# Optimization experiments

Measured on AMD Instinct MI355X. Metric: run time of the kernel, lower is better.

Reference implementation:

```python
import jax, jax.numpy as jnp
import numpy as np

B, N, V, D, L = 8, 2048, 256, 512, 6
H, DH = 8, 64
INNER = H * DH          # 512
WSZ = 128               # local attention window
NW = N // WSZ           # 16 windows (N multiple of WSZ -> autopad no-op)
FF = int(D * 4 * 2 / 3) # 1365 GEGLU inner dim
SCALE = DH ** -0.5
DPB = D // 2            # dynamic position bias MLP width


def _ln(x, g, b):
    m = x.mean(-1, keepdims=True)
    v = ((x - m) ** 2).mean(-1, keepdims=True)
    return (x - m) * jax.lax.rsqrt(v + 1e-5) * g + b


def _pos_emb(n, d):
    inv = 1.0 / (10000.0 ** (jnp.arange(0, d, 2, dtype=jnp.float32) / d))
    s = jnp.arange(n, dtype=jnp.float32)[:, None] * inv[None, :]
    return jnp.concatenate([jnp.sin(s), jnp.cos(s)], axis=-1)  # (n, d)


def _look(t, pad_val):
    # t: (..., NW, WSZ, c) -> (..., NW, 2*WSZ, c): [previous window, current window]
    prev = jnp.concatenate([jnp.full_like(t[..., :1, :, :], pad_val), t[..., :-1, :, :]], axis=-3)
    return jnp.concatenate([prev, t], axis=-2)


def _dpb_bias(w1, b1, w2, b2, w3, b3):
    # DynamicPositionBias(i=WSZ, j=2*WSZ) -> (H, WSZ, 2*WSZ)
    rel = jnp.arange(2 * WSZ, dtype=jnp.float32)[:, None]
    h = jax.nn.silu(rel @ w1 + b1)
    h = jax.nn.silu(h @ w2 + b2)
    tab = h @ w3 + b3                       # (2*WSZ, H)
    iseq = jnp.arange(WSZ, 2 * WSZ)
    jseq = jnp.arange(2 * WSZ)
    idx = jnp.abs(iseq[:, None] - jseq[None, :])  # (WSZ, 2*WSZ)
    return jnp.transpose(tab[idx], (2, 0, 1))


def setup_inputs():
    key = jax.random.key(0)
    ks = jax.random.split(key, 12)
    nrm = lambda k, shape, s=0.02: jax.random.normal(k, shape, dtype=jnp.float32) * s
    emb = nrm(ks[1], (V, D), 1.0).at[0].set(0.0)  # padding_idx=0 row zeroed
    return dict(
        x=jax.random.randint(ks[0], (B, N), 0, V),
        emb=emb,
        ln_attn_g=jnp.ones((L, D)), ln_attn_b=jnp.zeros((L, D)),
        w_qkv=nrm(ks[2], (L, D, 3 * INNER)),
        w_out=nrm(ks[3], (L, INNER, D)),
        ln_ff_g=jnp.ones((L, D)), ln_ff_b=jnp.zeros((L, D)),
        w_ff1=nrm(ks[4], (L, D, 2 * FF)),
        w_ff2=nrm(ks[5], (L, FF, D)),
        dpb_w1=nrm(ks[6], (1, DPB), 0.5), dpb_b1=jnp.zeros((DPB,)),
        dpb_w2=nrm(ks[7], (DPB, DPB), 0.05), dpb_b2=jnp.zeros((DPB,)),
        dpb_w3=nrm(ks[8], (DPB, H), 0.05), dpb_b3=jnp.zeros((H,)),
        ln_out_g=jnp.ones((D,)), ln_out_b=jnp.zeros((D,)),
        w_logits=nrm(ks[9], (D, D)),
    )


def _forward(x, emb, ln_attn_g, ln_attn_b, w_qkv, w_out, ln_ff_g, ln_ff_b,
             w_ff1, w_ff2, dpb_w1, dpb_b1, dpb_w2, dpb_b2, dpb_w3, dpb_b3,
             ln_out_g, ln_out_b, w_logits):
    mask = x != 0                                  # padding mask (B, N)
    h = emb[x] * mask[..., None] + _pos_emb(N, D)[None]
    bias = _dpb_bias(dpb_w1, dpb_b1, dpb_w2, dpb_b2, dpb_w3, dpb_b3)  # (H, w, 2w)
    pos = jnp.arange(N).reshape(NW, WSZ)
    kpos = _look(pos[None, :, :, None], -1)[0, :, :, 0]               # (NW, 2w)
    # causal mask + exact-windowsize clip + left pad mask (shared over batch/heads)
    inval = (pos[:, :, None] < kpos[:, None, :]) | (pos[:, :, None] > kpos[:, None, :] + WSZ) | (kpos[:, None, :] == -1)
    kmask = _look(mask.reshape(B, NW, WSZ)[..., None], False)[..., 0]  # (B, NW, 2w)
    neg = -jnp.finfo(jnp.float32).max

    def towin(t):  # (B, N, INNER) -> (B, H, NW, WSZ, DH)
        return t.reshape(B, N, H, DH).transpose(0, 2, 1, 3).reshape(B, H, NW, WSZ, DH)

    def layer(hx, p):
        lg, lb, wqkv, wout, fg, fb, w1, w2 = p
        # local windowed attention: look_backward=1, look_forward=0, causal
        z = _ln(hx, lg, lb)
        q, k, v = map(towin, jnp.split(z @ wqkv, 3, axis=-1))
        k2, v2 = _look(k, -1.0), _look(v, -1.0)   # pad_value=-1 (masked below)
        sim = jnp.einsum('bhwid,bhwjd->bhwij', q * SCALE, k2) + bias[None, :, None]
        sim = jnp.where(inval[None, None], neg, sim)
        sim = jnp.where(kmask[:, None, :, None, :], sim, neg)
        a = jax.nn.softmax(sim, axis=-1)
        o = jnp.einsum('bhwij,bhwjd->bhwid', a, v2)
        o = o.reshape(B, H, N, DH).transpose(0, 2, 1, 3).reshape(B, N, INNER)
        hx = hx + o @ wout
        # GEGLU feed-forward
        u = _ln(hx, fg, fb) @ w1
        a1, g1 = jnp.split(u, 2, axis=-1)
        hx = hx + (a1 * jax.nn.gelu(g1, approximate=False)) @ w2
        return hx, None

    h, _ = jax.lax.scan(layer, h, (ln_attn_g, ln_attn_b, w_qkv, w_out, ln_ff_g, ln_ff_b, w_ff1, w_ff2))
    return _ln(h, ln_out_g, ln_out_b) @ w_logits   # (B, N, D)


def reference(x, emb, ln_attn_g, ln_attn_b, w_qkv, w_out, ln_ff_g, ln_ff_b,
              w_ff1, w_ff2, dpb_w1, dpb_b1, dpb_w2, dpb_b2, dpb_w3, dpb_b3,
              ln_out_g, ln_out_b, w_logits):
    return _forward(x, emb, ln_attn_g, ln_attn_b, w_qkv, w_out, ln_ff_g, ln_ff_b,
                    w_ff1, w_ff2, dpb_w1, dpb_b1, dpb_w2, dpb_b2, dpb_w3, dpb_b3,
                    ln_out_g, ln_out_b, w_logits)
```

## Files before the change

### kernel.cpp

```cpp
#include <hip/hip_runtime.h>
#include <hip/hip_bf16.h>
#include <math.h>

typedef __hip_bfloat16 bf16;
typedef __attribute__((ext_vector_type(8))) short short8;
typedef __attribute__((ext_vector_type(4))) float floatx4;

#define NEG_MAX 3.402823466e38f

__device__ __forceinline__ void gload16(const void* g, void* l) {
  __builtin_amdgcn_global_load_lds(
      (const __attribute__((address_space(1))) unsigned int*)g,
      (__attribute__((address_space(3))) unsigned int*)l, 16, 0, 0);
}
__device__ __forceinline__ floatx4 mfma_bf16(short8 a, short8 b, floatx4 c) {
  return __builtin_amdgcn_mfma_f32_16x16x32_bf16(a, b, c, 0, 0, 0);
}

__global__ __launch_bounds__(256) void prep_w(const float* __restrict__ src,
                                              bf16* __restrict__ dst,
                                              int K, int N, int pK, int pN, int nl, int mode) {
  int idx = blockIdx.x * 256 + threadIdx.x;
  long total = (long)nl * pN * pK;
  if (idx >= total) return;
  int l = idx / (pN * pK);
  int r = idx % (pN * pK);
  int n = r / pK, k = r % pK;
  const float* s = src + (size_t)l * K * N;
  float v = 0.f;
  if (k < K) {
    int sc = -1;
    if (mode == 0) { if (n < N) sc = n; }
    else { if (n < 1365) sc = n; else if (n >= 1408 && n < 2773) sc = 1365 + (n - 1408); }
    if (sc >= 0) v = s[(size_t)k * N + sc];
  }
  dst[idx] = __float2bfloat16(v);
}

__global__ __launch_bounds__(256) void dpb_kernel(const float* w1, const float* b1,
                                                  const float* w2, const float* b2,
                                                  const float* w3, const float* b3,
                                                  float* __restrict__ tab) {
  __shared__ float h1[256];
  __shared__ float h2s[256];
  int t = blockIdx.x, e = threadIdx.x;
  float rel = (float)t;
  float a = rel * w1[e] + b1[e];
  h1[e] = a / (1.f + expf(-a));
  __syncthreads();
  float s = b2[e];
  for (int d = 0; d < 256; d++) s += h1[d] * w2[d * 256 + e];
  h2s[e] = s / (1.f + expf(-s));
  __syncthreads();
  if (e < 8) {
    float s2 = b3[e];
    for (int d = 0; d < 256; d++) s2 += h2s[d] * w3[d * 8 + e];
    tab[t * 8 + e] = s2;
  }
}

__global__ __launch_bounds__(256) void embed_kernel(const int* __restrict__ x,
                                                    const float* __restrict__ emb,
                                                    float* __restrict__ h) {
  int idx = blockIdx.x * 256 + threadIdx.x;
  int bn = idx >> 9, d = idx & 511;
  int n = bn & 2047;
  int xv = x[bn];
  float e = (xv != 0) ? emb[(size_t)xv * 512 + d] : 0.f;
  int k = d & 255;
  float inv = powf(10000.f, -(float)k * (1.f / 256.f));
  float s = (float)n * inv;
  float pe = (d < 256) ? sinf(s) : cosf(s);
  h[idx] = e + pe;
}

__global__ __launch_bounds__(256) void ln_kernel(const float* __restrict__ h,
                                                 const float* __restrict__ g,
                                                 const float* __restrict__ b,
                                                 bf16* __restrict__ z) {
  int wv = threadIdx.x >> 6, lane = threadIdx.x & 63;
  size_t row = (size_t)blockIdx.x * 4 + wv;
  const float* xr = h + row * 512;
  float v[8];
  float s = 0.f;
#pragma unroll
  for (int i = 0; i < 8; i++) { v[i] = xr[lane * 8 + i]; s += v[i]; }
#pragma unroll
  for (int o = 32; o > 0; o >>= 1) s += __shfl_xor(s, o);
  float mean = s * (1.f / 512.f);
  float q = 0.f;
#pragma unroll
  for (int i = 0; i < 8; i++) { float d = v[i] - mean; q += d * d; }
#pragma unroll
  for (int o = 32; o > 0; o >>= 1) q += __shfl_xor(q, o);
  float rs = rsqrtf(q * (1.f / 512.f) + 1e-5f);
  bf16* zr = z + row * 512;
#pragma unroll
  for (int i = 0; i < 8; i++) {
    int col = lane * 8 + i;
    float o2 = (v[i] - mean) * rs * g[col] + b[col];
    zr[col] = __float2bfloat16(o2);
  }
}

template <int EPI>
__global__ __launch_bounds__(256, 2) void gemm_kernel(const bf16* __restrict__ A,
                                                      const bf16* __restrict__ BT,
                                                      bf16* __restrict__ Cb,
                                                      float* __restrict__ Cf,
                                                      int Nsz, int Ksz) {
  __shared__ __align__(16) char smem[32768];
  const int tid = threadIdx.x, wv = tid >> 6, lane = tid & 63;
  const int lr = lane & 15, lg = lane >> 4;
  const int m0 = blockIdx.y * 128, n0 = blockIdx.x * 128;
  const int wm = (wv >> 1) * 64, wn = (wv & 1) * 64;
  const size_t Kb = (size_t)Ksz * 2;

  floatx4 acc[4][4];
#pragma unroll
  for (int i = 0; i < 4; i++)
#pragma unroll
    for (int j = 0; j < 4; j++)
#pragma unroll
      for (int r = 0; r < 4; r++) acc[i][j][r] = 0.f;

  for (int kt = 0; kt < Ksz; kt += 64) {
#pragma unroll
    for (int i = 0; i < 4; i++) {
      int off = i * 4096 + wv * 1024 + lane * 16;
      int row = off >> 7, colb = off & 127;
      int scol = colb ^ ((row & 7) << 4);
      gload16((const char*)A + (size_t)(m0 + row) * Kb + (size_t)kt * 2 + scol, smem + off);
    }
#pragma unroll
    for (int i = 0; i < 4; i++) {
      int off = i * 4096 + wv * 1024 + lane * 16;
      int row = off >> 7, colb = off & 127;
      int scol = colb ^ ((row & 7) << 4);
      gload16((const char*)BT + (size_t)(n0 + row) * Kb + (size_t)kt * 2 + scol,
              smem + 16384 + off);
    }
    __syncthreads();
#pragma unroll
    for (int kk = 0; kk < 64; kk += 32) {
      int kb = kk * 2 + lg * 16;
      short8 af[4], bfr[4];
#pragma unroll
      for (int mf = 0; mf < 4; mf++) {
        int row = wm + mf * 16 + lr;
        af[mf] = *(const short8*)(smem + row * 128 + (kb ^ ((row & 7) << 4)));
      }
#pragma unroll
      for (int nf = 0; nf < 4; nf++) {
        int row = wn + nf * 16 + lr;
        bfr[nf] = *(const short8*)(smem + 16384 + row * 128 + (kb ^ ((row & 7) << 4)));
      }
#pragma unroll
      for (int mf = 0; mf < 4; mf++)
#pragma unroll
        for (int nf = 0; nf < 4; nf++) acc[mf][nf] = mfma_bf16(af[mf], bfr[nf], acc[mf][nf]);
    }
    __syncthreads();
  }
#pragma unroll
  for (int mf = 0; mf < 4; mf++)
#pragma unroll
    for (int nf = 0; nf < 4; nf++)
#pragma unroll
      for (int r = 0; r < 4; r++) {
        int row = m0 + wm + mf * 16 + lg * 4 + r;
        int col = n0 + wn + nf * 16 + lr;
        float v = acc[mf][nf][r];
        size_t idx = (size_t)row * Nsz + col;
        if (EPI == 0) {
          Cb[idx] = __float2bfloat16(v);
        } else if (EPI == 1) {
          Cf[idx] += v;
        } else if (EPI == 2) {
          float a = __bfloat162float(Cb[idx]);
          float ge = 0.5f * v * (1.f + erff(v * 0.70710678118654752f));
          Cb[idx] = __float2bfloat16(a * ge);
        } else {
          Cf[idx] = v;
        }
      }
}

__global__ __launch_bounds__(256) void attn_kernel(const bf16* __restrict__ qkv,
                                                   const int* __restrict__ x,
                                                   const float* __restrict__ tab,
                                                   bf16* __restrict__ ob) {
  __shared__ __align__(16) char smem[65536];
  float* km = (float*)smem;
  float* tabh = (float*)(smem + 1024);
  const int w2 = blockIdx.x, hh = blockIdx.y, b = blockIdx.z;
  const int w = w2 >> 1, qh = (w2 & 1) * 64;
  const int tid = threadIdx.x, wv = tid >> 6, lane = tid & 63;
  const int lr = lane & 15, lg = lane >> 4;
  const size_t qrow0 = (size_t)b * 2048 + (size_t)w * 128;

  for (int c = tid; c < 2048; c += 256) {
    int j = c >> 3, d0 = (c & 7) * 8;
    short8 vv;
    if (w == 0 && j < 128) {
#pragma unroll
      for (int t2 = 0; t2 < 8; t2++) vv[t2] = (short)0xBF80;
    } else {
      size_t gj = qrow0 + j - 128;
      vv = *(const short8*)(qkv + gj * 1536 + 1024 + hh * 64 + d0);
    }
#pragma unroll
    for (int t2 = 0; t2 < 8; t2++) {
      int d = d0 + t2;
      *(unsigned short*)(smem + 32768 + d * 512 + ((j * 2) ^ ((d & 7) << 4))) =
          (unsigned short)vv[t2];
    }
  }
  {
    tabh[tid] = tab[tid * 8 + hh];
    int j = tid;
    float kmv;
    if (w == 0 && j < 128) kmv = 0.f;
    else kmv = (x[qrow0 + j - 128] != 0) ? 1.f : 0.f;
    km[j] = kmv;
  }
  __syncthreads();

  floatx4 sim[16];
#pragma unroll
  for (int nf = 0; nf < 16; nf++)
#pragma unroll
    for (int r = 0; r < 4; r++) sim[nf][r] = 0.f;
#pragma unroll
  for (int kk = 0; kk < 64; kk += 32) {
    size_t qr = qrow0 + qh + wv * 16 + lr;
    short8 aq = *(const short8*)(qkv + qr * 1536 + hh * 64 + kk + lg * 8);
#pragma unroll
    for (int nf = 0; nf < 16; nf++) {
      int j = nf * 16 + lr;
      size_t gj = (w == 0 && j < 128) ? qrow0 : (qrow0 + j - 128);
      short8 bk = *(const short8*)(qkv + gj * 1536 + 512 + hh * 64 + kk + lg * 8);
      sim[nf] = mfma_bf16(aq, bk, sim[nf]);
    }
  }
  float inv_s[4];
#pragma unroll
  for (int r = 0; r < 4; r++) {
    int qi = qh + wv * 16 + lg * 4 + r;
    float mmax = -NEG_MAX;
#pragma unroll
    for (int nf = 0; nf < 16; nf++) {
      int j = nf * 16 + lr;
      int di = 128 + qi - j;
      if (di < 0) di = -di;
      float val = sim[nf][r] * 0.125f + tabh[di];
      bool valid = ((j < 128) ? (qi <= j) : (j - 128 <= qi)) && (km[j] > 0.5f);
      float mv = valid ? val : -NEG_MAX;
      sim[nf][r] = mv;
      mmax = fmaxf(mmax, mv);
    }
#pragma unroll
    for (int o = 8; o > 0; o >>= 1) mmax = fmaxf(mmax, __shfl_xor(mmax, o));
    float s = 0.f;
#pragma unroll
    for (int nf = 0; nf < 16; nf++) {
      float e = expf(sim[nf][r] - mmax);
      sim[nf][r] = e;
      s += e;
    }
#pragma unroll
    for (int o = 8; o > 0; o >>= 1) s += __shfl_xor(s, o);
    inv_s[r] = 1.f / s;
  }
  __syncthreads();
#pragma unroll
  for (int nf = 0; nf < 16; nf++)
#pragma unroll
    for (int r = 0; r < 4; r++) {
      int qi = wv * 16 + lg * 4 + r;
      int j = nf * 16 + lr;
      *(unsigned short*)(smem + qi * 512 + ((j * 2) ^ ((qi & 7) << 4))) =
          __bfloat16_as_ushort(__float2bfloat16(sim[nf][r] * inv_s[r]));
    }
  __syncthreads();
  floatx4 oacc[4];
#pragma unroll
  for (int nf = 0; nf < 4; nf++)
#pragma unroll
    for (int r = 0; r < 4; r++) oacc[nf][r] = 0.f;
#pragma unroll
  for (int kk = 0; kk < 256; kk += 32) {
    int kb = kk * 2 + lg * 16;
    int row = wv * 16 + lr;
    short8 pa = *(const short8*)(smem + row * 512 + (kb ^ ((row & 7) << 4)));
#pragma unroll
    for (int nf = 0; nf < 4; nf++) {
      int d = nf * 16 + lr;
      short8 bv = *(const short8*)(smem + 32768 + d * 512 + (kb ^ ((d & 7) << 4)));
      oacc[nf] = mfma_bf16(pa, bv, oacc[nf]);
    }
  }
#pragma unroll
  for (int nf = 0; nf < 4; nf++)
#pragma unroll
    for (int r = 0; r < 4; r++) {
      size_t n = qrow0 + qh + wv * 16 + lg * 4 + r;
      ob[n * 512 + hh * 64 + nf * 16 + lr] = __float2bfloat16(oacc[nf][r]);
    }
}

extern "C" void kernel_launch(void* const* d_in, const int* in_sizes, int n_in,
                              void* d_out, int out_size, void* d_ws, size_t ws_size,
                              hipStream_t stream) {
  const int* x = (const int*)d_in[0];
  const float* emb = (const float*)d_in[1];
  const float* lag = (const float*)d_in[2];
  const float* lab = (const float*)d_in[3];
  const float* wqkv = (const float*)d_in[4];
  const float* wout = (const float*)d_in[5];
  const float* lfg = (const float*)d_in[6];
  const float* lfb = (const float*)d_in[7];
  const float* wff1 = (const float*)d_in[8];
  const float* wff2 = (const float*)d_in[9];
  const float* dw1 = (const float*)d_in[10];
  const float* db1 = (const float*)d_in[11];
  const float* dw2 = (const float*)d_in[12];
  const float* db2 = (const float*)d_in[13];
  const float* dw3 = (const float*)d_in[14];
  const float* db3 = (const float*)d_in[15];
  const float* log_g = (const float*)d_in[16];
  const float* log_b = (const float*)d_in[17];
  const float* wlog = (const float*)d_in[18];

  char* ws = (char*)d_ws;
  size_t off = 0;
  float* h = (float*)(ws + off); off += (size_t)16384 * 512 * 4;
  bf16* z = (bf16*)(ws + off); off += (size_t)16384 * 512 * 2;
  bf16* ob = z;
  bf16* big = (bf16*)(ws + off); off += (size_t)16384 * 1536 * 2;
  bf16* qkvT = (bf16*)(ws + off); off += (size_t)6 * 1536 * 512 * 2;
  bf16* woutT = (bf16*)(ws + off); off += (size_t)6 * 512 * 512 * 2;
  bf16* ff1T = (bf16*)(ws + off); off += (size_t)6 * 2816 * 512 * 2;
  bf16* ff2T = (bf16*)(ws + off); off += (size_t)6 * 512 * 1408 * 2;
  bf16* logT = (bf16*)(ws + off); off += (size_t)512 * 512 * 2;
  float* tab = (float*)(ws + off); off += (size_t)256 * 8 * 4;

  auto cdiv = [](long t) { return (int)((t + 255) / 256); };

  prep_w<<<cdiv(6L * 1536 * 512), 256, 0, stream>>>(wqkv, qkvT, 512, 1536, 512, 1536, 6, 0);
  prep_w<<<cdiv(6L * 512 * 512), 256, 0, stream>>>(wout, woutT, 512, 512, 512, 512, 6, 0);
  prep_w<<<cdiv(6L * 2816 * 512), 256, 0, stream>>>(wff1, ff1T, 512, 2730, 512, 2816, 6, 1);
  prep_w<<<cdiv(6L * 512 * 1408), 256, 0, stream>>>(wff2, ff2T, 1365, 512, 1408, 512, 6, 0);
  prep_w<<<cdiv(512L * 512), 256, 0, stream>>>(wlog, logT, 512, 512, 512, 512, 1, 0);
  dpb_kernel<<<256, 256, 0, stream>>>(dw1, db1, dw2, db2, dw3, db3, tab);
  embed_kernel<<<32768, 256, 0, stream>>>(x, emb, h);

  for (int l = 0; l < 6; l++) {
    ln_kernel<<<4096, 256, 0, stream>>>(h, lag + l * 512, lab + l * 512, z);
    gemm_kernel<0><<<dim3(12, 128), 256, 0, stream>>>(z, qkvT + (size_t)l * 1536 * 512,
                                                      big, nullptr, 1536, 512);
    attn_kernel<<<dim3(32, 8, 8), 256, 0, stream>>>(big, x, tab, ob);
    gemm_kernel<1><<<dim3(4, 128), 256, 0, stream>>>(ob, woutT + (size_t)l * 512 * 512,
                                                     nullptr, h, 512, 512);
    ln_kernel<<<4096, 256, 0, stream>>>(h, lfg + l * 512, lfb + l * 512, z);
    gemm_kernel<0><<<dim3(11, 128), 256, 0, stream>>>(z, ff1T + (size_t)l * 2816 * 512,
                                                      big, nullptr, 1408, 512);
    gemm_kernel<2><<<dim3(11, 128), 256, 0, stream>>>(
        z, ff1T + (size_t)l * 2816 * 512 + (size_t)1408 * 512, big, nullptr, 1408, 512);
    gemm_kernel<1><<<dim3(4, 128), 256, 0, stream>>>(big, ff2T + (size_t)l * 512 * 1408,
                                                     nullptr, h, 512, 1408);
  }
  ln_kernel<<<4096, 256, 0, stream>>>(h, log_g, log_b, z);
  gemm_kernel<3><<<dim3(4, 128), 256, 0, stream>>>(z, logT, nullptr, (float*)d_out, 512, 512);
}
```

Before: 2.196 ms.

## Transpose QK^T in attention so softmax is per-lane with half-size P staging

The attention kernel swaps the QK^T MFMA operands so each lane holds one query row across keys. Row max and sum then need only two cross-lane shuffles instead of per-row butterfly reductions, and exp uses the fast intrinsic. Unnormalized probabilities are packed as bf16 and staged in two 128-key halves. This cuts shared memory from 64KB to 50KB, which may allow more resident blocks, and normalization moves to the output write. The cost is extra barriers, and storing unnormalized probabilities in bf16 slightly changes rounding.

```diff
diff --git a/kernel.cpp b/kernel.cpp
--- a/kernel.cpp
+++ b/kernel.cpp
@@ -190,9 +190,9 @@
                                                    const int* __restrict__ x,
                                                    const float* __restrict__ tab,
                                                    bf16* __restrict__ ob) {
-  __shared__ __align__(16) char smem[65536];
-  float* km = (float*)smem;
-  float* tabh = (float*)(smem + 1024);
+  __shared__ __align__(16) char smem[51200];
+  float* km = (float*)(smem + 49152);
+  float* tabh = (float*)(smem + 50176);
   const int w2 = blockIdx.x, hh = blockIdx.y, b = blockIdx.z;
   const int w = w2 >> 1, qh = (w2 & 1) * 64;
   const int tid = threadIdx.x, wv = tid >> 6, lane = tid & 63;
@@ -212,7 +212,7 @@
 #pragma unroll
     for (int t2 = 0; t2 < 8; t2++) {
       int d = d0 + t2;
-      *(unsigned short*)(smem + 32768 + d * 512 + ((j * 2) ^ ((d & 7) << 4))) =
+      *(unsigned short*)(smem + 16384 + d * 512 + ((j * 2) ^ ((d & 7) << 4))) =
           (unsigned short)vv[t2];
     }
   }
@@ -234,78 +234,90 @@
 #pragma unroll
   for (int kk = 0; kk < 64; kk += 32) {
     size_t qr = qrow0 + qh + wv * 16 + lr;
-    short8 aq = *(const short8*)(qkv + qr * 1536 + hh * 64 + kk + lg * 8);
+    short8 bq = *(const short8*)(qkv + qr * 1536 + hh * 64 + kk + lg * 8);
 #pragma unroll
     for (int nf = 0; nf < 16; nf++) {
       int j = nf * 16 + lr;
       size_t gj = (w == 0 && j < 128) ? qrow0 : (qrow0 + j - 128);
-      short8 bk = *(const short8*)(qkv + gj * 1536 + 512 + hh * 64 + kk + lg * 8);
-      sim[nf] = mfma_bf16(aq, bk, sim[nf]);
-    }
-  }
-  float inv_s[4];
-#pragma unroll
-  for (int r = 0; r < 4; r++) {
-    int qi = qh + wv * 16 + lg * 4 + r;
-    float mmax = -NEG_MAX;
-#pragma unroll
-    for (int nf = 0; nf < 16; nf++) {
-      int j = nf * 16 + lr;
-      int di = 128 + qi - j;
+      short8 ak = *(const short8*)(qkv + gj * 1536 + 512 + hh * 64 + kk + lg * 8);
+      sim[nf] = mfma_bf16(ak, bq, sim[nf]);
+    }
+  }
+  const int qi = qh + wv * 16 + lr;
+  float mmax = -NEG_MAX;
+#pragma unroll
+  for (int nf = 0; nf < 16; nf++)
+#pragma unroll
+    for (int r = 0; r < 4; r++) {
+      int jj = nf * 16 + lg * 4 + r;
+      int di = 128 + qi - jj;
       if (di < 0) di = -di;
       float val = sim[nf][r] * 0.125f + tabh[di];
-      bool valid = ((j < 128) ? (qi <= j) : (j - 128 <= qi)) && (km[j] > 0.5f);
+      bool causal = (nf < 8) ? (qi <= jj) : (jj - 128 <= qi);
+      bool valid = causal && (km[jj] > 0.5f);
       float mv = valid ? val : -NEG_MAX;
       sim[nf][r] = mv;
       mmax = fmaxf(mmax, mv);
     }
-#pragma unroll
-    for (int o = 8; o > 0; o >>= 1) mmax = fmaxf(mmax, __shfl_xor(mmax, o));
-    float s = 0.f;
-#pragma unroll
-    for (int nf = 0; nf < 16; nf++) {
-      float e = expf(sim[nf][r] - mmax);
+  mmax = fmaxf(mmax, __shfl_xor(mmax, 16));
+  mmax = fmaxf(mmax, __shfl_xor(mmax, 32));
+  float lsum = 0.f;
+#pragma unroll
+  for (int nf = 0; nf < 16; nf++)
+#pragma unroll
+    for (int r = 0; r < 4; r++) {
+      float e = __expf(sim[nf][r] - mmax);
       sim[nf][r] = e;
-      s += e;
-    }
-#pragma unroll
-    for (int o = 8; o > 0; o >>= 1) s += __shfl_xor(s, o);
-    inv_s[r] = 1.f / s;
-  }
-  __syncthreads();
-#pragma unroll
-  for (int nf = 0; nf < 16; nf++)
-#pragma unroll
-    for (int r = 0; r < 4; r++) {
-      int qi = wv * 16 + lg * 4 + r;
-      int j = nf * 16 + lr;
-      *(unsigned short*)(smem + qi * 512 + ((j * 2) ^ ((qi & 7) << 4))) =
-          __bfloat16_as_ushort(__float2bfloat16(sim[nf][r] * inv_s[r]));
-    }
-  __syncthreads();
+      lsum += e;
+    }
+  lsum += __shfl_xor(lsum, 16);
+  lsum += __shfl_xor(lsum, 32);
+  float inv_l = 1.f / lsum;
+
   floatx4 oacc[4];
 #pragma unroll
   for (int nf = 0; nf < 4; nf++)
 #pragma unroll
     for (int r = 0; r < 4; r++) oacc[nf][r] = 0.f;
-#pragma unroll
-  for (int kk = 0; kk < 256; kk += 32) {
-    int kb = kk * 2 + lg * 16;
-    int row = wv * 16 + lr;
-    short8 pa = *(const short8*)(smem + row * 512 + (kb ^ ((row & 7) << 4)));
-#pragma unroll
-    for (int nf = 0; nf < 4; nf++) {
-      int d = nf * 16 + lr;
-      short8 bv = *(const short8*)(smem + 32768 + d * 512 + (kb ^ ((d & 7) << 4)));
-      oacc[nf] = mfma_bf16(pa, bv, oacc[nf]);
-    }
-  }
+
+  const int ql = wv * 16 + lr;
+#pragma unroll
+  for (int t = 0; t < 2; t++) {
+#pragma unroll
+    for (int nfl = 0; nfl < 8; nfl++) {
+      int nf = t * 8 + nfl;
+      unsigned int lo = (unsigned int)__bfloat16_as_ushort(__float2bfloat16(sim[nf][0])) |
+                        ((unsigned int)__bfloat16_as_ushort(__float2bfloat16(sim[nf][1])) << 16);
+      unsigned int hi = (unsigned int)__bfloat16_as_ushort(__float2bfloat16(sim[nf][2])) |
+                        ((unsigned int)__bfloat16_as_ushort(__float2bfloat16(sim[nf][3])) << 16);
+      uint2 pk; pk.x = lo; pk.y = hi;
+      int bo = nfl * 32 + lg * 8;
+      *(uint2*)(smem + ql * 256 + (bo ^ ((ql & 7) << 4))) = pk;
+    }
+    __syncthreads();
+#pragma unroll
+    for (int kkl = 0; kkl < 128; kkl += 32) {
+      int bo = kkl * 2 + lg * 16;
+      short8 pa = *(const short8*)(smem + ql * 256 + (bo ^ ((ql & 7) << 4)));
+      int vb = t * 256 + bo;
+#pragma unroll
+      for (int nf = 0; nf < 4; nf++) {
+        int d = nf * 16 + lr;
+        short8 bv = *(const short8*)(smem + 16384 + d * 512 + (vb ^ ((d & 7) << 4)));
+        oacc[nf] = mfma_bf16(pa, bv, oacc[nf]);
+      }
+    }
+    __syncthreads();
+  }
+  float invq[4];
+#pragma unroll
+  for (int r = 0; r < 4; r++) invq[r] = __shfl(inv_l, (lane & 48) | (lg * 4 + r));
 #pragma unroll
   for (int nf = 0; nf < 4; nf++)
 #pragma unroll
     for (int r = 0; r < 4; r++) {
       size_t n = qrow0 + qh + wv * 16 + lg * 4 + r;
-      ob[n * 512 + hh * 64 + nf * 16 + lr] = __float2bfloat16(oacc[nf][r]);
+      ob[n * 512 + hh * 64 + nf * 16 + lr] = __float2bfloat16(oacc[nf][r] * invq[r]);
     }
 }
 
```

After: 2.132 ms. 2.9% less time.
